# Optimization experiments

Hardware: AMD Instinct MI355X
Metric: run time of the kernel (lower is better)

## Reference

```python
import jax, jax.numpy as jnp
import numpy as np

BN_EPS = 1e-5


def setup_inputs() -> dict:
    key = jax.random.key(0)
    ks = jax.random.split(key, 6)
    B, C, N = 8, 256, 4096
    C4 = C // 4
    return {
        "x": jax.random.normal(ks[0], (B, C, N), dtype=jnp.float32),
        "w_qk": jax.random.normal(ks[1], (C4, C), dtype=jnp.float32) * 0.05,  # shared q/k weight
        "w_v": jax.random.normal(ks[2], (C, C), dtype=jnp.float32) * 0.05,
        "b_v": jax.random.normal(ks[3], (C,), dtype=jnp.float32) * 0.05,
        "w_t": jax.random.normal(ks[4], (C, C), dtype=jnp.float32) * 0.05,
        "b_t": jax.random.normal(ks[5], (C,), dtype=jnp.float32) * 0.05,
        "gamma": jnp.ones((C,), dtype=jnp.float32),
        "beta": jnp.zeros((C,), dtype=jnp.float32),
        "run_mean": jnp.zeros((C,), dtype=jnp.float32),
        "run_var": jnp.ones((C,), dtype=jnp.float32),
    }


def reference(x, w_qk, w_v, b_v, w_t, b_t, gamma, beta, run_mean, run_var):
    # x: [B, C, N]; 1x1 Conv1d == channel matmul.
    x_q = jnp.einsum('oc,bcn->bno', w_qk, x)               # [B, N, C/4]
    x_k = jnp.einsum('oc,bcn->bon', w_qk, x)               # [B, C/4, N]
    energy = jnp.einsum('bno,bom->bnm', x_q, x_k)          # [B, N, N], NO 1/sqrt(d) scaling
    attn = jax.nn.softmax(energy, axis=-1)                 # softmax over last dim only
    x_v = jnp.einsum('oc,bcn->bon', w_v, x) + b_v[None, :, None]  # [B, C, N]
    x_r = jnp.einsum('bcn,bnm->bcm', x_v, attn)            # V @ attn (right-multiply, no transpose)
    t = jnp.einsum('oc,bcn->bon', w_t, x - x_r) + b_t[None, :, None]
    # BatchNorm1d (inference): per-channel affine with running stats
    inv = gamma / jnp.sqrt(run_var + BN_EPS)
    bn = t * inv[None, :, None] + (beta - run_mean * inv)[None, :, None]
    return x + jnp.maximum(bn, 0.0)
```

## Files before the change

### kernel.cpp

```cpp
#include <hip/hip_runtime.h>

#define Bb 8
#define Cc 256
#define C4 64
#define Nn 4096

typedef _Float16 half8 __attribute__((ext_vector_type(8)));
typedef float f32x4 __attribute__((ext_vector_type(4)));
typedef unsigned int u32;

__device__ __forceinline__ f32x4 fz4() {
  f32x4 z; z[0] = 0.f; z[1] = 0.f; z[2] = 0.f; z[3] = 0.f; return z;
}
__device__ __forceinline__ f32x4 mfma16(half8 a, half8 b, f32x4 c) {
  return __builtin_amdgcn_mfma_f32_16x16x32_f16(a, b, c, 0, 0, 0);
}
__device__ __forceinline__ u32 pkrtz(float a, float b) {
  typedef __fp16 h2n __attribute__((ext_vector_type(2)));
  h2n h = __builtin_amdgcn_cvt_pkrtz(a, b);
  return __builtin_bit_cast(u32, h);
}
__device__ __forceinline__ float ex2(float x) {
  float r;
  asm("v_exp_f32 %0, %1" : "=v"(r) : "v"(x));
  return r;
}


__global__ void k0_weights(const float* __restrict__ wqk, const float* __restrict__ wv,
                           const float* __restrict__ wt,
                           _Float16* __restrict__ wqkh, _Float16* __restrict__ wqkl,
                           _Float16* __restrict__ wvf, _Float16* __restrict__ wtf) {
  int idx = blockIdx.x * 256 + threadIdx.x;
  if (idx < C4 * Cc) {
    int o = idx >> 8, c = idx & 255;
    float f = wqk[idx] * 1.2011224087864498f;
    _Float16 h = (_Float16)f;
    int off = ((((o >> 4) * 8 + (c >> 5)) * 4 + ((c >> 3) & 3)) * 16 + (o & 15)) * 8 + (c & 7);
    wqkh[off] = h;
    wqkl[off] = (_Float16)(f - (float)h);
  }
  if (idx < Cc * Cc) {
    int o = idx >> 8, k = idx & 255;
    int off = ((((o >> 4) * 8 + (k >> 5)) * 4 + ((k >> 3) & 3)) * 16 + (o & 15)) * 8 + (k & 7);
    wvf[off] = (_Float16)wv[idx];
    wtf[off] = (_Float16)wt[idx];
  }
}

__global__ __launch_bounds__(512) void k23_qkv(
    const float* __restrict__ x,
    const _Float16* __restrict__ wqkh, const _Float16* __restrict__ wqkl,
    const _Float16* __restrict__ wvf, const float* __restrict__ bv,
    _Float16* __restrict__ qkf, _Float16* __restrict__ xvf) {
  __shared__ _Float16 xh[64 * 264];
  const int bid = blockIdx.x;
  const int b = bid & 7, n0 = (bid >> 3) * 64, tid = threadIdx.x;
  {
    const int cc = tid >> 3, nn = (tid & 7) * 8;
    #pragma unroll
    for (int ph = 0; ph < 4; ++ph) {
      int c = cc + ph * 64;
      const float* src = x + ((size_t)(b * Cc + c)) * Nn + n0 + nn;
      float4 v0 = *(const float4*)(src);
      float4 v1 = *(const float4*)(src + 4);
      float vv[8] = {v0.x, v0.y, v0.z, v0.w, v1.x, v1.y, v1.z, v1.w};
      #pragma unroll
      for (int j = 0; j < 8; ++j) xh[(nn + j) * 264 + c] = (_Float16)vv[j];
    }
  }
  __syncthreads();
  const int w = tid >> 6, lane = tid & 63, l15 = lane & 15, l4 = lane >> 4;
  {
    const int fn = w >> 1, ob = (w & 1) * 32;
    f32x4 acc[2] = {fz4(), fz4()};
    #pragma unroll
    for (int kb = 0; kb < 8; ++kb) {
      half8 ah = *(const half8*)(xh + (fn * 16 + l15) * 264 + kb * 32 + l4 * 8);
      #pragma unroll
      for (int f = 0; f < 2; ++f) {
        const int ot = (ob >> 4) + f;
        half8 bh = *(const half8*)((const char*)wqkh + (ot * 8 + kb) * 1024 + lane * 16);
        half8 bl = *(const half8*)((const char*)wqkl + (ot * 8 + kb) * 1024 + lane * 16);
        acc[f] = mfma16(ah, bh, acc[f]);
        acc[f] = mfma16(ah, bl, acc[f]);
      }
    }
    #pragma unroll
    for (int f = 0; f < 2; ++f)
      #pragma unroll
      for (int i = 0; i < 4; ++i) {
        const int n = n0 + fn * 16 + l4 * 4 + i;
        const int o = ob + f * 16 + l15;
        int off = ((((b * 256 + (n >> 4)) * 2 + (o >> 5)) * 4 + ((o >> 3) & 3)) * 16 +
                   (n & 15)) * 8 + (o & 7);
        qkf[off] = (_Float16)acc[f][i];
      }
  }
  {
    const int cb = w * 32;
    f32x4 acc[2][4];
    #pragma unroll
    for (int a = 0; a < 2; ++a)
      #pragma unroll
      for (int q = 0; q < 4; ++q) acc[a][q] = fz4();
    #pragma unroll
    for (int kb = 0; kb < 8; ++kb) {
      half8 bfr[4];
      #pragma unroll
      for (int fnb = 0; fnb < 4; ++fnb)
        bfr[fnb] = *(const half8*)(xh + (fnb * 16 + l15) * 264 + kb * 32 + l4 * 8);
      #pragma unroll
      for (int fc = 0; fc < 2; ++fc) {
        const int ct = (cb >> 4) + fc;
        half8 a = *(const half8*)((const char*)wvf + (ct * 8 + kb) * 1024 + lane * 16);
        #pragma unroll
        for (int fnb = 0; fnb < 4; ++fnb)
          acc[fc][fnb] = mfma16(a, bfr[fnb], acc[fc][fnb]);
      }
    }
    #pragma unroll
    for (int fc = 0; fc < 2; ++fc)
      #pragma unroll
      for (int fnb = 0; fnb < 4; ++fnb)
        #pragma unroll
        for (int i = 0; i < 4; ++i) {
          const int c = cb + fc * 16 + l4 * 4 + i;
          const int n = n0 + fnb * 16 + l15;
          int off = ((((b * 16 + (c >> 4)) * 128 + (n >> 5)) * 4 + ((n >> 3) & 3)) * 16 +
                     (c & 15)) * 8 + (n & 7);
          xvf[off] = (_Float16)(acc[fc][fnb][i] + bv[c]);
        }
  }
}

__global__ __launch_bounds__(512, 4) void k4_stats(
    const _Float16* __restrict__ qkf, float* __restrict__ stats) {
  __shared__ float red[64][8];
  const int bid = blockIdx.x;
  const int b = bid & 7, n0 = (bid >> 3) * 64, tid = threadIdx.x;
  const int w = tid >> 6, lane = tid & 63, l15 = lane & 15, l4 = lane >> 4;
  const char* qbt = (const char*)qkf + (size_t)b * 524288;

  half8 qn_r[2][4];
  #pragma unroll
  for (int kb = 0; kb < 2; ++kb)
    #pragma unroll
    for (int fn = 0; fn < 4; ++fn)
      qn_r[kb][fn] = *(const half8*)(qbt + (((n0 >> 4) + fn) * 2 + kb) * 1024 + lane * 16);

  const char* qp = qbt + w * 2048 + lane * 16;
  half8 qa0 = *(const half8*)qp;
  half8 qa1 = *(const half8*)(qp + 1024);

  float sm[4] = {0.f, 0.f, 0.f, 0.f};
  for (int it = 0; it < 32; ++it) {
    f32x4 g[4] = {fz4(), fz4(), fz4(), fz4()};
    #pragma unroll
    for (int fn = 0; fn < 4; ++fn) g[fn] = mfma16(qa0, qn_r[0][fn], g[fn]);
    #pragma unroll
    for (int fn = 0; fn < 4; ++fn) g[fn] = mfma16(qa1, qn_r[1][fn], g[fn]);
    if (it < 31) qp += 16384;
    qa0 = *(const half8*)qp;
    qa1 = *(const half8*)(qp + 1024);
    #pragma unroll
    for (int fn = 0; fn < 4; ++fn)
      #pragma unroll
      for (int i = 0; i < 4; ++i)
        sm[fn] += ex2(g[fn][i] - 32.0f);
  }
  #pragma unroll
  for (int fn = 0; fn < 4; ++fn) {
    sm[fn] += __shfl_xor(sm[fn], 16, 64);
    sm[fn] += __shfl_xor(sm[fn], 32, 64);
  }
  if (l4 == 0) {
    #pragma unroll
    for (int fn = 0; fn < 4; ++fn) red[fn * 16 + l15][w] = sm[fn];
  }
  __syncthreads();
  if (tid < 64) {
    float t = 0.f;
    #pragma unroll
    for (int j = 0; j < 8; ++j) t += red[tid][j];
    stats[(size_t)b * Nn + n0 + tid] = 32.0f + log2f(t);
  }
}

__global__ __launch_bounds__(512, 2) void k5_main(
    const float* __restrict__ x,
    const _Float16* __restrict__ qkf, const _Float16* __restrict__ xvf,
    const float* __restrict__ stats,
    const _Float16* __restrict__ wtf, const float* __restrict__ bt,
    const float* __restrict__ gamma, const float* __restrict__ beta,
    const float* __restrict__ rmean, const float* __restrict__ rvar,
    float* __restrict__ out) {
  __shared__ __align__(16) char smem[69632];
  const int bid = blockIdx.x;
  const int b = bid & 7, m0 = (bid >> 3) * 128, tid = threadIdx.x;
  const int w = tid >> 6, lane = tid & 63, l15 = lane & 15, l4 = lane >> 4;
  const int wa = w >> 2;
  const int wb = w & 3;
  const size_t bq = (size_t)b * Nn;
  const char* qkt = (const char*)qkf + (size_t)b * 524288;
  const char* xvt = (const char*)xvf + (size_t)b * 2097152;
  const int key = l15 & 7;
  float* anL = (float*)smem;

  half8 qm_r[2][4];
  #pragma unroll
  for (int kb = 0; kb < 2; ++kb)
    #pragma unroll
    for (int fm = 0; fm < 4; ++fm)
      qm_r[kb][fm] = *(const half8*)(qkt + ((((m0 >> 4) + wa * 4 + fm) * 2) + kb) * 1024 +
                                     lane * 16);

  const char* ah_base = qkt + (wb * 2) * 1024 + (size_t)lane * 16;
  const char* xb_base = xvt + (size_t)(wb * 4) * 131072 + (size_t)lane * 16;

  f32x4 acc[4][4];
  #pragma unroll
  for (int a = 0; a < 4; ++a)
    #pragma unroll
    for (int q = 0; q < 4; ++q) acc[a][q] = fz4();

  #pragma unroll
  for (int j = 0; j < 2; ++j)
    ((float4*)anL)[tid + 512 * j] = ((const float4*)(stats + bq))[tid + 512 * j];
  half8 ahA[2], ahB[2], xbA[4][2], xbB[4][2];
  #pragma unroll
  for (int kb = 0; kb < 2; ++kb) ahA[kb] = *(const half8*)(ah_base + kb * 1024);
  #pragma unroll
  for (int fc = 0; fc < 4; ++fc)
    #pragma unroll
    for (int kb = 0; kb < 2; ++kb)
      xbA[fc][kb] = *(const half8*)(xb_base + fc * 131072 + kb * 1024);
  __syncthreads();

#define K5_STEP(P, AH_CUR, AH_NXT, XB_CUR, XB_NXT)                                  \
  {                                                                                \
    const int it = it2 * 2 + (P);                                                  \
                 \
    {                                                                              \
      const char* ahs = ah_base + (size_t)(it + 1) * 8192;                         \
      _Pragma("unroll") for (int kb = 0; kb < 2; ++kb)                             \
          AH_NXT[kb] = *(const half8*)(ahs + kb * 1024);                           \
      const char* xbs = xb_base + (size_t)(it + 1) * 2048;                         \
      _Pragma("unroll") for (int fc = 0; fc < 4; ++fc)                             \
        _Pragma("unroll") for (int kb = 0; kb < 2; ++kb)                           \
            XB_NXT[fc][kb] = *(const half8*)(xbs + fc * 131072 + kb * 1024);       \
    }                                                                              \
                                                               \
    f32x4 g[4] = {fz4(), fz4(), fz4(), fz4()};                                     \
    _Pragma("unroll") for (int kb = 0; kb < 2; ++kb)                               \
      _Pragma("unroll") for (int fm = 0; fm < 4; ++fm)                             \
          g[fm] = mfma16(AH_CUR[kb], qm_r[kb][fm], g[fm]);                         \
                                  \
    char* PTp = smem + 16384 + ((P) << 14);                                        \
    {                                                                              \
      float4 an = *(const float4*)(anL + it * 64 + wb * 16 + l4 * 4);              \
      _Pragma("unroll") for (int fm = 0; fm < 4; ++fm) {                           \
        uint2 pk;                                                                  \
        pk.x = pkrtz(ex2(g[fm][0] - an.x), ex2(g[fm][1] - an.y));                  \
        pk.y = pkrtz(ex2(g[fm][2] - an.z), ex2(g[fm][3] - an.w));                  \
        *(uint2*)(PTp + (wa * 64 + fm * 16 + l15) * 128 +                          \
                  ((wb * 32 + l4 * 8) ^ (key << 4))) = pk;                         \
      }                                                                            \
    }                                                                              \
                                                     \
    asm volatile("s_waitcnt lgkmcnt(0)" ::: "memory");                             \
    __builtin_amdgcn_sched_barrier(0);                                             \
    __builtin_amdgcn_s_barrier();                                                  \
                                      \
    __builtin_amdgcn_s_setprio(1);                                                 \
    _Pragma("unroll") for (int kb = 0; kb < 2; ++kb) {                             \
      half8 pa[4];                                                                 \
      _Pragma("unroll") for (int fm = 0; fm < 4; ++fm)                             \
          pa[fm] = *(const half8*)(PTp + (wa * 64 + fm * 16 + l15) * 128 +         \
                                   (((kb * 4 + l4) ^ key) * 16));                  \
      _Pragma("unroll") for (int fm = 0; fm < 4; ++fm)                             \
        _Pragma("unroll") for (int fc = 0; fc < 4; ++fc)                           \
            acc[fm][fc] = mfma16(pa[fm], XB_CUR[fc][kb], acc[fm][fc]);             \
    }                                                                              \
    __builtin_amdgcn_s_setprio(0);                                                 \
  }

  for (int it2 = 0; it2 < 32; ++it2) {
    K5_STEP(0, ahA, ahB, xbA, xbB)
    K5_STEP(1, ahB, ahA, xbB, xbA)
  }
#undef K5_STEP
  asm volatile("s_waitcnt lgkmcnt(0)" ::: "memory");
  __builtin_amdgcn_sched_barrier(0);
  __builtin_amdgcn_s_barrier();

  _Float16* st = (_Float16*)smem;
  #pragma unroll
  for (int fm = 0; fm < 4; ++fm)
    #pragma unroll
    for (int fc = 0; fc < 4; ++fc) {
      int c = wb * 64 + fc * 16 + l15;
      int mb = wa * 64 + fm * 16 + l4 * 4;
      const float* xp = x + ((size_t)b * Cc + c) * Nn + m0 + mb;
      float4 v = *(const float4*)xp;
      float vv[4] = {v.x, v.y, v.z, v.w};
      #pragma unroll
      for (int i = 0; i < 4; ++i)
        st[(mb + i) * 264 + c] = (_Float16)(vv[i] - acc[fm][fc][i]);
    }
  __syncthreads();
  {
    const int ob = wb * 64, mh = wa * 64;
    f32x4 t[4][4];
    #pragma unroll
    for (int a = 0; a < 4; ++a)
      #pragma unroll
      for (int q = 0; q < 4; ++q) t[a][q] = fz4();
    #pragma unroll
    for (int kb = 0; kb < 8; ++kb) {
      half8 bfr[4];
      #pragma unroll
      for (int fm2 = 0; fm2 < 4; ++fm2)
        bfr[fm2] = *(const half8*)(st + (mh + fm2 * 16 + l15) * 264 + kb * 32 + l4 * 8);
      #pragma unroll
      for (int fo = 0; fo < 4; ++fo) {
        const int ot = (ob >> 4) + fo;
        half8 a = *(const half8*)((const char*)wtf + (ot * 8 + kb) * 1024 + lane * 16);
        #pragma unroll
        for (int fm2 = 0; fm2 < 4; ++fm2)
          t[fo][fm2] = mfma16(a, bfr[fm2], t[fo][fm2]);
      }
    }
    #pragma unroll
    for (int fo = 0; fo < 4; ++fo)
      #pragma unroll
      for (int i = 0; i < 4; ++i) {
        const int o = ob + fo * 16 + l4 * 4 + i;
        const float inv = gamma[o] * rsqrtf(rvar[o] + 1e-5f);
        const float addv = beta[o] - rmean[o] * inv;
        const float btv = bt[o];
        #pragma unroll
        for (int fm2 = 0; fm2 < 4; ++fm2) {
          const int m = m0 + mh + fm2 * 16 + l15;
          float tv = t[fo][fm2][i] + btv;
          float bn = tv * inv + addv;
          float xr = x[((size_t)b * Cc + o) * Nn + m];
          out[((size_t)b * Cc + o) * Nn + m] = xr + fmaxf(bn, 0.0f);
        }
      }
  }
}

extern "C" void kernel_launch(void* const* d_in, const int* in_sizes, int n_in,
                              void* d_out, int out_size, void* d_ws, size_t ws_size,
                              hipStream_t stream) {
  const float* x = (const float*)d_in[0];
  const float* wqk = (const float*)d_in[1];
  const float* wv = (const float*)d_in[2];
  const float* bv = (const float*)d_in[3];
  const float* wt = (const float*)d_in[4];
  const float* bt = (const float*)d_in[5];
  const float* gamma = (const float*)d_in[6];
  const float* beta = (const float*)d_in[7];
  const float* rmean = (const float*)d_in[8];
  const float* rvar = (const float*)d_in[9];
  float* out = (float*)d_out;

  char* ws = (char*)d_ws;
  size_t off = 0;
  auto alloc = [&](size_t nb) {
    char* p = ws + off;
    off += (nb + 255) & ~(size_t)255;
    return p;
  };
  _Float16* qkf = (_Float16*)alloc((size_t)Bb * Nn * C4 * 2);
  _Float16* xvf = (_Float16*)alloc((size_t)Bb * Cc * Nn * 2);
  float* stats = (float*)alloc((size_t)Bb * Nn * 4);
  _Float16* wqkh = (_Float16*)alloc((size_t)C4 * Cc * 2);
  _Float16* wqkl = (_Float16*)alloc((size_t)C4 * Cc * 2);
  _Float16* wvf = (_Float16*)alloc((size_t)Cc * Cc * 2);
  _Float16* wtf = (_Float16*)alloc((size_t)Cc * Cc * 2);

  k0_weights<<<dim3(256), dim3(256), 0, stream>>>(wqk, wv, wt, wqkh, wqkl, wvf, wtf);
  k23_qkv<<<dim3(512), dim3(512), 0, stream>>>(x, wqkh, wqkl, wvf, bv, qkf, xvf);
  k4_stats<<<dim3(512), dim3(512), 0, stream>>>(qkf, stats);
  k5_main<<<dim3(256), dim3(512), 0, stream>>>(x, qkf, xvf, stats, wtf, bt,
                                               gamma, beta, rmean, rvar, out);
}
```

Baseline: 140.2 us.

## Software-pipeline PV matmul one step behind QK/exp with wave-staggered ordering

Restructures the attention main loop so each step computes the QK scores and exp into one LDS buffer while running the P·V MFMAs on the previous step's buffer. Half the waves (wa==1) do PV before the QK/exp and the other half after, so the two phases overlap across waves. One barrier per step now covers both phases, and a prologue and epilogue handle pipeline fill and drain. The XB register loads are now issued for the current step rather than one ahead, which shortens their prefetch distance and may expose global-load latency.

Measured after the change: 151.5 us. 8.1% more time.

```diff
diff --git a/kernel.cpp b/kernel.cpp
--- a/kernel.cpp
+++ b/kernel.cpp
@@ -227,69 +227,74 @@
   #pragma unroll
   for (int j = 0; j < 2; ++j)
     ((float4*)anL)[tid + 512 * j] = ((const float4*)(stats + bq))[tid + 512 * j];
-  half8 ahA[2], ahB[2], xbA[4][2], xbB[4][2];
+  half8 ahA[2] = {}, ahB[2] = {}, xbA[4][2] = {}, xbB[4][2] = {};
   #pragma unroll
   for (int kb = 0; kb < 2; ++kb) ahA[kb] = *(const half8*)(ah_base + kb * 1024);
-  #pragma unroll
-  for (int fc = 0; fc < 4; ++fc)
-    #pragma unroll
-    for (int kb = 0; kb < 2; ++kb)
-      xbA[fc][kb] = *(const half8*)(xb_base + fc * 131072 + kb * 1024);
   __syncthreads();
 
-#define K5_STEP(P, AH_CUR, AH_NXT, XB_CUR, XB_NXT)                                  \
+#define K5_PV(PTR_, XB_)                                                            \
+  {                                                                                \
+    __builtin_amdgcn_s_setprio(1);                                                 \
+    _Pragma("unroll") for (int kb = 0; kb < 2; ++kb) {                             \
+      half8 pa[4];                                                                 \
+      _Pragma("unroll") for (int fm = 0; fm < 4; ++fm)                             \
+          pa[fm] = *(const half8*)((PTR_) + (wa * 64 + fm * 16 + l15) * 128 +      \
+                                   (((kb * 4 + l4) ^ key) * 16));                  \
+      _Pragma("unroll") for (int fm = 0; fm < 4; ++fm)                             \
+        _Pragma("unroll") for (int fc = 0; fc < 4; ++fc)                           \
+            acc[fm][fc] = mfma16(pa[fm], (XB_)[fc][kb], acc[fm][fc]);              \
+    }                                                                              \
+    __builtin_amdgcn_s_setprio(0);                                                 \
+  }
+
+#define K5_STEP(P, FIRST, AH_CUR, AH_NXT, XB_THIS, XB_PREV)                         \
   {                                                                                \
     const int it = it2 * 2 + (P);                                                  \
-                 \
+    float4 an = *(const float4*)(anL + it * 64 + wb * 16 + l4 * 4);                \
     {                                                                              \
       const char* ahs = ah_base + (size_t)(it + 1) * 8192;                         \
       _Pragma("unroll") for (int kb = 0; kb < 2; ++kb)                             \
           AH_NXT[kb] = *(const half8*)(ahs + kb * 1024);                           \
-      const char* xbs = xb_base + (size_t)(it + 1) * 2048;                         \
+      const char* xbs = xb_base + (size_t)it * 2048;                               \
       _Pragma("unroll") for (int fc = 0; fc < 4; ++fc)                             \
         _Pragma("unroll") for (int kb = 0; kb < 2; ++kb)                           \
-            XB_NXT[fc][kb] = *(const half8*)(xbs + fc * 131072 + kb * 1024);       \
+            XB_THIS[fc][kb] = *(const half8*)(xbs + fc * 131072 + kb * 1024);      \
     }                                                                              \
-                                                               \
+    char* PTw = smem + 16384 + ((P) << 14);                                        \
+    char* PTr = smem + 16384 + (((P) ^ 1) << 14);                                  \
+    if (!(FIRST) && wa == 1) K5_PV(PTr, XB_PREV);                                  \
     f32x4 g[4] = {fz4(), fz4(), fz4(), fz4()};                                     \
     _Pragma("unroll") for (int kb = 0; kb < 2; ++kb)                               \
       _Pragma("unroll") for (int fm = 0; fm < 4; ++fm)                             \
           g[fm] = mfma16(AH_CUR[kb], qm_r[kb][fm], g[fm]);                         \
-                                  \
-    char* PTp = smem + 16384 + ((P) << 14);                                        \
-    {                                                                              \
-      float4 an = *(const float4*)(anL + it * 64 + wb * 16 + l4 * 4);              \
-      _Pragma("unroll") for (int fm = 0; fm < 4; ++fm) {                           \
-        uint2 pk;                                                                  \
-        pk.x = pkrtz(ex2(g[fm][0] - an.x), ex2(g[fm][1] - an.y));                  \
-        pk.y = pkrtz(ex2(g[fm][2] - an.z), ex2(g[fm][3] - an.w));                  \
-        *(uint2*)(PTp + (wa * 64 + fm * 16 + l15) * 128 +                          \
-                  ((wb * 32 + l4 * 8) ^ (key << 4))) = pk;                         \
-      }                                                                            \
+    _Pragma("unroll") for (int fm = 0; fm < 4; ++fm) {                             \
+      uint2 pk;                                                                    \
+      pk.x = pkrtz(ex2(g[fm][0] - an.x), ex2(g[fm][1] - an.y));                    \
+      pk.y = pkrtz(ex2(g[fm][2] - an.z), ex2(g[fm][3] - an.w));                    \
+      *(uint2*)(PTw + (wa * 64 + fm * 16 + l15) * 128 +                            \
+                ((wb * 32 + l4 * 8) ^ (key << 4))) = pk;                           \
     }                                                                              \
-                                                     \
+    if (!(FIRST) && wa == 0) K5_PV(PTr, XB_PREV);                                  \
     asm volatile("s_waitcnt lgkmcnt(0)" ::: "memory");                             \
     __builtin_amdgcn_sched_barrier(0);                                             \
     __builtin_amdgcn_s_barrier();                                                  \
-                                      \
-    __builtin_amdgcn_s_setprio(1);                                                 \
-    _Pragma("unroll") for (int kb = 0; kb < 2; ++kb) {                             \
-      half8 pa[4];                                                                 \
-      _Pragma("unroll") for (int fm = 0; fm < 4; ++fm)                             \
-          pa[fm] = *(const half8*)(PTp + (wa * 64 + fm * 16 + l15) * 128 +         \
-                                   (((kb * 4 + l4) ^ key) * 16));                  \
-      _Pragma("unroll") for (int fm = 0; fm < 4; ++fm)                             \
-        _Pragma("unroll") for (int fc = 0; fc < 4; ++fc)                           \
-            acc[fm][fc] = mfma16(pa[fm], XB_CUR[fc][kb], acc[fm][fc]);             \
-    }                                                                              \
-    __builtin_amdgcn_s_setprio(0);                                                 \
-  }
-
-  for (int it2 = 0; it2 < 32; ++it2) {
-    K5_STEP(0, ahA, ahB, xbA, xbB)
-    K5_STEP(1, ahB, ahA, xbB, xbA)
+  }
+
+  {
+    const int it2 = 0;
+    K5_STEP(0, 1, ahA, ahB, xbA, xbB)
+    K5_STEP(1, 0, ahB, ahA, xbB, xbA)
+  }
+  for (int it2 = 1; it2 < 32; ++it2) {
+    K5_STEP(0, 0, ahA, ahB, xbA, xbB)
+    K5_STEP(1, 0, ahB, ahA, xbB, xbA)
+  }
+  {
+    char* PTr = smem + 16384 + 16384;
+    K5_PV(PTr, xbB);
   }
 #undef K5_STEP
+#undef K5_PV
   asm volatile("s_waitcnt lgkmcnt(0)" ::: "memory");
   __builtin_amdgcn_sched_barrier(0);
   __builtin_amdgcn_s_barrier();
```
